# Optimization experiments

Measured on AMD Instinct MI355X. Metric: run time of the kernel, lower is better.

## Reference

```python
import jax, jax.numpy as jnp
import numpy as np
import math

K = 3
PAD = K // 2
C = 128          # out_channels
IN_CH = 256      # in_channels (concat of x2 and upsampled x1)
MOD_CH = 512     # modul_channels
SCALE = 1.0 / math.sqrt(C * K * K)


def conv2d(x, w, b=None, padding=0, groups=1):
    # x: [N, Cin, H, W], w: [Cout, Cin/groups, kh, kw]
    out = jax.lax.conv_general_dilated(
        x, w, window_strides=(1, 1),
        padding=[(padding, padding), (padding, padding)],
        feature_group_count=groups)
    if b is not None:
        out = out + b[None, :, None, None]
    return out


def leaky(x):
    return jnp.where(x >= 0, x, 0.1 * x)


def setup_inputs() -> dict:
    key = jax.random.key(0)
    ks = jax.random.split(key, 16)
    B, H, W = 8, 128, 128
    inp = {
        'x1': jax.random.normal(ks[0], (B, 128, H // 2, W // 2), jnp.float32),
        'x2': jax.random.normal(ks[1], (B, 128, H, W), jnp.float32),
        'xg': jax.random.normal(ks[2], (B, MOD_CH, 1, 1), jnp.float32),
        # modulation 1x1 conv
        'w_mod': jax.random.normal(ks[3], (C, MOD_CH, 1, 1), jnp.float32) * 0.05,
        'b_mod': jnp.ones((C,), jnp.float32),
        # styled weight parameter
        'w_style': jax.random.normal(ks[4], (1, C, C, K, K), jnp.float32),
        # ResBlock params
        'w_bottle': jax.random.normal(ks[5], (C, IN_CH, 1, 1), jnp.float32) * 0.05,
        'b_bottle': jnp.zeros((C,), jnp.float32),
        'w_dc1': jax.random.normal(ks[6], (C, C, 3, 3), jnp.float32) * 0.03,
        'b_dc1': jnp.zeros((C,), jnp.float32),
        'w_dc2': jax.random.normal(ks[7], (C, C, 3, 3), jnp.float32) * 0.03,
        'b_dc2': jnp.zeros((C,), jnp.float32),
        # conv_last
        'w_last': jax.random.normal(ks[8], (C, C, 3, 3), jnp.float32) * 0.03,
        'b_last': jnp.zeros((C,), jnp.float32),
    }
    return inp


def reference(x1, x2, xg, w_mod, b_mod, w_style, w_bottle, b_bottle,
              w_dc1, b_dc1, w_dc2, b_dc2, w_last, b_last):
    B, _, H, W = x2.shape
    # style modulation: [B, C, 1, 1] -> [B, 1, C, 1, 1]
    style = conv2d(xg, w_mod, b_mod).reshape(B, 1, C, 1, 1)
    weight = SCALE * w_style * style                         # [B, C, C, K, K]
    demod = jax.lax.rsqrt(jnp.sum(weight * weight, axis=(2, 3, 4)) + 1e-8)
    weight = weight * demod[:, :, None, None, None]
    weight = weight.reshape(B * C, C, K, K)
    x1u = jax.image.resize(x1, (B, x1.shape[1], H, W), method='bilinear')
    x = jnp.concatenate([x2, x1u], axis=1)                   # [B, IN_CH, H, W]
    # ResBlock
    x = conv2d(x, w_bottle, b_bottle)
    y = leaky(conv2d(x, w_dc1, b_dc1, padding=1))
    y = conv2d(y, w_dc2, b_dc2, padding=1)
    x = (y + x) / math.sqrt(2)
    # per-sample modulated grouped conv
    x_in = x.reshape(1, B * C, H, W)
    x_global = conv2d(x_in, weight, padding=PAD, groups=B).reshape(B, C, H, W)
    out = leaky(conv2d(x_global, w_last, b_last, padding=1))
    return out
```

## Files before the change

kernel.cpp:

```cpp
#include <hip/hip_runtime.h>
#include <stdint.h>

typedef _Float16 f16x8 __attribute__((ext_vector_type(8)));
typedef float    f32x4 __attribute__((ext_vector_type(4)));

#define DEVFN static __device__ __forceinline__

DEVFN unsigned short f2hu(float f) {
  _Float16 h = (_Float16)f;
  return __builtin_bit_cast(unsigned short, h);
}
DEVFN float h2f(unsigned short u) {
  return (float)__builtin_bit_cast(_Float16, u);
}
DEVFN float lrelu(float v) { return v >= 0.f ? v : 0.1f * v; }

DEVFN void gload16(const void* g, const void* l) {
  __builtin_amdgcn_global_load_lds(
      (const __attribute__((address_space(1))) void*)(uintptr_t)g,
      (__attribute__((address_space(3))) void*)(uint32_t)(uintptr_t)l,
      16, 0, 0);
}

static constexpr float SCALE_C = 0.029462782549439476f;

static constexpr size_t OFF_SIN  = 0;
static constexpr size_t OFF_DS   = 4096;
static constexpr size_t OFF_ZERO = 8192;
static constexpr size_t OFF_W2   = 12288;
static constexpr size_t OFF_WPK  = 77824;
static constexpr size_t OFF_WB   = OFF_WPK + 4ull * 147456ull * 2ull;
static constexpr size_t OFF_XCAT = OFF_WB + 65536;
static constexpr size_t OFF_XB   = OFF_XCAT + 8ull * 16384ull * 256ull * 2ull;
static constexpr size_t OFF_Y1   = OFF_XB + 8ull * 16384ull * 128ull * 2ull;

__global__ __launch_bounds__(256) void prep1_kernel(
    const float* __restrict__ xg, const float* __restrict__ w_mod,
    const float* __restrict__ b_mod, const float* __restrict__ w_style,
    const float* __restrict__ w_dc1, const float* __restrict__ w_dc2,
    const float* __restrict__ w_last, const float* __restrict__ w_bottle,
    unsigned short* __restrict__ wpk, unsigned short* __restrict__ wb,
    float* __restrict__ s_in, float* __restrict__ w2buf,
    float* __restrict__ zerob) {
  const int idx = (int)blockIdx.x * 256 + (int)threadIdx.x;
  if (idx < 589824) {
    const int t  = idx / 147456;
    const int e  = idx - t * 147456;
    const int co = e / 1152;
    const int r  = e - co * 1152;
    const int tap = r >> 7;
    const int ci  = r & 127;
    const float* src = (t == 0) ? w_dc1 : (t == 1) ? w_dc2 : (t == 2) ? w_style : w_last;
    wpk[idx] = f2hu(src[(size_t)(co * 128 + ci) * 9 + tap]);
    return;
  }
  int j = idx - 589824;
  if (j < 32768) { wb[j] = f2hu(w_bottle[j]); return; }
  j -= 32768;
  if (j < 65536) {
    const int pair = j >> 6, ln = j & 63;
    const int b = pair >> 7, ci = pair & 127;
    float st = 0.f;
    for (int m = ln; m < 512; m += 64) st += xg[b * 512 + m] * w_mod[ci * 512 + m];
    for (int off = 32; off > 0; off >>= 1) st += __shfl_down(st, off);
    if (ln == 0) s_in[pair] = st + b_mod[ci];
    return;
  }
  j -= 65536;
  if (j < 16384) {
    float acc = 0.f;
#pragma unroll
    for (int t = 0; t < 9; ++t) { float w = w_style[(size_t)j * 9 + t]; acc += w * w; }
    w2buf[j] = acc;
    return;
  }
  j -= 16384;
  if (j < 64) zerob[j] = 0.f;
}

__global__ __launch_bounds__(256) void prep2_kernel(
    const float* __restrict__ s_in, const float* __restrict__ w2buf,
    float* __restrict__ dscale) {
  const int j = (int)blockIdx.x * 256 + (int)threadIdx.x;
  const int pair = j >> 6, ln = j & 63;
  const int b = pair >> 7, co = pair & 127;
  const float s0 = s_in[b * 128 + ln];
  const float s1 = s_in[b * 128 + 64 + ln];
  float acc = s0 * s0 * w2buf[co * 128 + ln] + s1 * s1 * w2buf[co * 128 + 64 + ln];
  for (int off = 32; off > 0; off >>= 1) acc += __shfl_down(acc, off);
  if (ln == 0)
    dscale[pair] = SCALE_C * rsqrtf(SCALE_C * SCALE_C * acc + 1e-8f);
}

__global__ __launch_bounds__(256) void upcat_kernel(
    const float* __restrict__ x2, const float* __restrict__ x1,
    unsigned short* __restrict__ xcat) {
  __shared__ unsigned short lds[256 * 128];
  const int bid = (int)blockIdx.x;
  const int b = bid >> 7, h = bid & 127;
  const int tid = (int)threadIdx.x;
  const int crow = tid >> 5, wq = tid & 31;

  for (int it = 0; it < 16; ++it) {
    const int c = it * 8 + crow;
    const float4 v = *(const float4*)(x2 + ((size_t)(b * 128 + c) * 16384 + h * 128 + wq * 4));
    ushort4 u;
    u.x = f2hu(v.x); u.y = f2hu(v.y); u.z = f2hu(v.z); u.w = f2hu(v.w);
    *(ushort4*)(&lds[c * 128 + wq * 4]) = u;
  }
  const int m = h >> 1;
  const bool oddh = (h & 1);
  const int ly = oddh ? m : m - 1;
  const float fy = oddh ? 0.25f : 0.75f;
  const int y0 = ly < 0 ? 0 : ly;
  const int y1 = (ly + 1) > 63 ? 63 : (ly + 1);
  for (int it = 0; it < 16; ++it) {
    const int c = it * 8 + crow;
    const float* r0 = x1 + ((size_t)(b * 128 + c) * 4096 + y0 * 64);
    const float* r1 = x1 + ((size_t)(b * 128 + c) * 4096 + y1 * 64);
    ushort4 u;
    unsigned short* up = (unsigned short*)&u;
#pragma unroll
    for (int k = 0; k < 4; ++k) {
      const int w = wq * 4 + k;
      const int n = w >> 1;
      const bool oddw = (w & 1);
      const int lx = oddw ? n : n - 1;
      const float fx = oddw ? 0.25f : 0.75f;
      const int x0i = lx < 0 ? 0 : lx;
      const int x1i = (lx + 1) > 63 ? 63 : (lx + 1);
      const float vy0 = (1.f - fx) * r0[x0i] + fx * r0[x1i];
      const float vy1 = (1.f - fx) * r1[x0i] + fx * r1[x1i];
      up[k] = f2hu((1.f - fy) * vy0 + fy * vy1);
    }
    *(ushort4*)(&lds[(128 + c) * 128 + wq * 4]) = u;
  }
  __syncthreads();
  const int w = tid >> 1;
  const int c0 = (tid & 1) << 7;
  unsigned short* dst = xcat + ((size_t)((b * 128 + h) * 128 + w)) * 256 + c0;
  for (int i0 = 0; i0 < 128; i0 += 8) {
    unsigned int a0 = lds[(c0 + i0 + 0) * 128 + w];
    unsigned int a1 = lds[(c0 + i0 + 1) * 128 + w];
    unsigned int a2 = lds[(c0 + i0 + 2) * 128 + w];
    unsigned int a3 = lds[(c0 + i0 + 3) * 128 + w];
    unsigned int a4 = lds[(c0 + i0 + 4) * 128 + w];
    unsigned int a5 = lds[(c0 + i0 + 5) * 128 + w];
    unsigned int a6 = lds[(c0 + i0 + 6) * 128 + w];
    unsigned int a7 = lds[(c0 + i0 + 7) * 128 + w];
    uint4 q;
    q.x = a0 | (a1 << 16); q.y = a2 | (a3 << 16);
    q.z = a4 | (a5 << 16); q.w = a6 | (a7 << 16);
    *(uint4*)(dst + i0) = q;
  }
}

template <int TAPS, int CTOT, int EPI>
__global__ __launch_bounds__(512, 1) void conv_mfma(
    const unsigned short* __restrict__ Xin, const unsigned short* __restrict__ Wpk,
    const float* __restrict__ bias, const float* __restrict__ sstyle,
    const unsigned short* __restrict__ resid, unsigned short* __restrict__ outb,
    float* __restrict__ outf, const float* __restrict__ zerob) {
  constexpr int ROWS = (TAPS > 1) ? 4 : 2;
  constexpr int WSL  = (TAPS > 1) ? 130 : 128;
  constexpr int XSLOTS = ROWS * WSL * 4;
  constexpr int WSLOTS = 128 * TAPS * 4;
  constexpr int XBYTES = XSLOTS * 16;
  constexpr int NCB = CTOT / 32;

  __shared__ char smem[XBYTES + WSLOTS * 16];

  const int bid0 = (int)blockIdx.x;
  const int bid  = (bid0 & 7) * 64 + (bid0 >> 3);
  const int b  = bid >> 6;
  const int h0 = (bid & 63) << 1;

  const int tid = (int)threadIdx.x;
  const int wid = tid >> 6, lane = tid & 63;
  const int wm = wid >> 1, wn = wid & 1;
  const int g = lane >> 4, l15 = lane & 15;

  f32x4 acc[4][4] = {};

  const size_t imgbase = (size_t)b * 16384 * CTOT;

  for (int cb = 0; cb < NCB; ++cb) {
    const int ci0 = cb * 32;
    __syncthreads();
    for (int sb = wid * 64; sb < XSLOTS; sb += 512) {
      const int s = sb + lane;
      const int rws = s >> 2, cpr = s & 3;
      const int row = rws / WSL;
      const int ws  = rws - row * WSL;
      const int c   = cpr ^ (ws & 3);
      const void* src;
      if (TAPS > 1) {
        const int hrow = h0 + row - 1;
        const int w = ws - 1;
        src = (hrow >= 0 && hrow < 128 && w >= 0 && w < 128)
                  ? (const void*)(Xin + imgbase + (size_t)(hrow * 128 + w) * CTOT + ci0 + c * 8)
                  : (const void*)zerob;
      } else {
        src = Xin + imgbase + (size_t)((h0 + row) * 128 + ws) * CTOT + ci0 + c * 8;
      }
      if ((XSLOTS & 511) == 0 || s < XSLOTS) gload16(src, smem + sb * 16);
    }
    for (int sb = wid * 64; sb < WSLOTS; sb += 512) {
      const int s = sb + lane;
      const int co  = s / (TAPS * 4);
      const int rem = s - co * (TAPS * 4);
      const int tap = rem >> 2, cpr = rem & 3;
      const int c = cpr ^ (co & 3);
      gload16(Wpk + (size_t)(co * TAPS + tap) * CTOT + ci0 + c * 8,
              smem + XBYTES + sb * 16);
    }
    __syncthreads();
#pragma unroll
    for (int tap = 0; tap < TAPS; ++tap) {
      f16x8 af[4], bf[4];
#pragma unroll
      for (int mf = 0; mf < 4; ++mf) {
        const int mm = wm * 64 + mf * 16 + l15;
        const int r_out = mm >> 7, w = mm & 127;
        const int rrow = (TAPS > 1) ? (r_out + tap / 3) : r_out;
        const int ws   = (TAPS > 1) ? (w + tap % 3) : w;
        af[mf] = *(const f16x8*)(smem + ((rrow * WSL + ws) * 4 + (g ^ (ws & 3))) * 16);
      }
#pragma unroll
      for (int nf = 0; nf < 4; ++nf) {
        const int co = wn * 64 + nf * 16 + l15;
        bf[nf] = *(const f16x8*)(smem + XBYTES + ((co * TAPS + tap) * 4 + (g ^ (co & 3))) * 16);
      }
#pragma unroll
      for (int mf = 0; mf < 4; ++mf)
#pragma unroll
        for (int nf = 0; nf < 4; ++nf)
          acc[mf][nf] = __builtin_amdgcn_mfma_f32_16x16x32_f16(af[mf], bf[nf], acc[mf][nf], 0, 0, 0);
    }
  }

  const int hrow = h0 + (wm >> 1);
  const int wb0  = (wm & 1) * 64;
#pragma unroll
  for (int nf = 0; nf < 4; ++nf) {
    const int co = wn * 64 + nf * 16 + l15;
    float bv = 0.f;
    if (EPI == 0 || EPI == 1 || EPI == 2 || EPI == 4) bv = bias[co];
    float sv = 0.f;
    if (EPI == 2 || EPI == 3) sv = sstyle[b * 128 + co];
#pragma unroll
    for (int mf = 0; mf < 4; ++mf) {
      const int wcol = wb0 + mf * 16 + 4 * g;
      const f32x4 v = acc[mf][nf];
      if (EPI == 4) {
        float4 o;
        o.x = lrelu(v[0] + bv); o.y = lrelu(v[1] + bv);
        o.z = lrelu(v[2] + bv); o.w = lrelu(v[3] + bv);
        *(float4*)(outf + ((size_t)(b * 128 + co) * 16384 + hrow * 128 + wcol)) = o;
      } else {
#pragma unroll
        for (int r = 0; r < 4; ++r) {
          const size_t pidx = ((size_t)((b * 128 + hrow) * 128 + (wcol + r))) * 128 + co;
          float x = v[r];
          if (EPI == 0) x += bv;
          if (EPI == 1) x = lrelu(x + bv);
          if (EPI == 2) x = (x + bv + h2f(resid[pidx])) * 0.70710678118654752f * sv;
          if (EPI == 3) x *= sv;
          outb[pidx] = f2hu(x);
        }
      }
    }
  }
}

extern "C" void kernel_launch(void* const* d_in, const int* in_sizes, int n_in,
                              void* d_out, int out_size, void* d_ws, size_t ws_size,
                              hipStream_t stream) {
  (void)in_sizes; (void)n_in; (void)out_size; (void)ws_size;
  const float* x1       = (const float*)d_in[0];
  const float* x2       = (const float*)d_in[1];
  const float* xg       = (const float*)d_in[2];
  const float* w_mod    = (const float*)d_in[3];
  const float* b_mod    = (const float*)d_in[4];
  const float* w_style  = (const float*)d_in[5];
  const float* w_bottle = (const float*)d_in[6];
  const float* b_bottle = (const float*)d_in[7];
  const float* w_dc1    = (const float*)d_in[8];
  const float* b_dc1    = (const float*)d_in[9];
  const float* w_dc2    = (const float*)d_in[10];
  const float* b_dc2    = (const float*)d_in[11];
  const float* w_last   = (const float*)d_in[12];
  const float* b_last   = (const float*)d_in[13];
  float* out = (float*)d_out;

  char* ws = (char*)d_ws;
  float* s_in           = (float*)(ws + OFF_SIN);
  float* dscale         = (float*)(ws + OFF_DS);
  float* zerob          = (float*)(ws + OFF_ZERO);
  float* w2buf          = (float*)(ws + OFF_W2);
  unsigned short* wpk   = (unsigned short*)(ws + OFF_WPK);
  unsigned short* wb    = (unsigned short*)(ws + OFF_WB);
  unsigned short* xcat  = (unsigned short*)(ws + OFF_XCAT);
  unsigned short* xb    = (unsigned short*)(ws + OFF_XB);
  unsigned short* y1    = (unsigned short*)(ws + OFF_Y1);
  unsigned short* xr    = xcat;
  unsigned short* xglob = xb;

  prep1_kernel<<<2753, 256, 0, stream>>>(xg, w_mod, b_mod, w_style, w_dc1, w_dc2,
                                         w_last, w_bottle, wpk, wb, s_in, w2buf, zerob);
  prep2_kernel<<<256, 256, 0, stream>>>(s_in, w2buf, dscale);
  upcat_kernel<<<1024, 256, 0, stream>>>(x2, x1, xcat);
  conv_mfma<1, 256, 0><<<512, 512, 0, stream>>>(xcat, wb, b_bottle, nullptr, nullptr, xb, nullptr, zerob);
  conv_mfma<9, 128, 1><<<512, 512, 0, stream>>>(xb, wpk, b_dc1, nullptr, nullptr, y1, nullptr, zerob);
  conv_mfma<9, 128, 2><<<512, 512, 0, stream>>>(y1, wpk + 147456, b_dc2, s_in, xb, xr, nullptr, zerob);
  conv_mfma<9, 128, 3><<<512, 512, 0, stream>>>(xr, wpk + 2 * 147456, nullptr, dscale, nullptr, xglob, nullptr, zerob);
  conv_mfma<9, 128, 4><<<512, 512, 0, stream>>>(xglob, wpk + 3 * 147456, b_last, nullptr, nullptr, nullptr, out, zerob);
}
```

Measured before the change: 423.3 us.

## Double-buffer conv input tiles, enlarge row tiles, stream weights from global

The conv kernel now processes four output rows per block (256 blocks) and double-buffers the input tile in LDS. The next channel block is prefetched with global_load_lds while MFMAs run on the current one, using explicit vmcnt waits and barriers. For 3x3 convs, weights are read straight from global/cache into registers instead of being staged in LDS; the 1x1 bottleneck preloads its full weight matrix into LDS once. The upsample/concat kernel is split into half-width tiles with a padded transpose buffer. The extra overlap and reuse aim to hide load latency, at the cost of hand-tuned waitcnt counts, higher register pressure and only 256 blocks.

```diff
diff --git a/kernel.cpp b/kernel.cpp
--- a/kernel.cpp
+++ b/kernel.cpp
@@ -75,7 +75,7 @@
     return;
   }
   j -= 16384;
-  if (j < 64) zerob[j] = 0.f;
+  if (j < 128) zerob[j] = 0.f;
 }
 
 __global__ __launch_bounds__(256) void prep2_kernel(
@@ -92,175 +92,203 @@
     dscale[pair] = SCALE_C * rsqrtf(SCALE_C * SCALE_C * acc + 1e-8f);
 }
 
-__global__ __launch_bounds__(256) void upcat_kernel(
+__global__ __launch_bounds__(256) void upcat2_kernel(
     const float* __restrict__ x2, const float* __restrict__ x1,
     unsigned short* __restrict__ xcat) {
-  __shared__ unsigned short lds[256 * 128];
+  __shared__ unsigned short lt[256][65];
   const int bid = (int)blockIdx.x;
-  const int b = bid >> 7, h = bid & 127;
+  const int b = bid >> 8, h = (bid >> 1) & 127, w0 = (bid & 1) << 6;
   const int tid = (int)threadIdx.x;
-  const int crow = tid >> 5, wq = tid & 31;
-
-  for (int it = 0; it < 16; ++it) {
-    const int c = it * 8 + crow;
-    const float4 v = *(const float4*)(x2 + ((size_t)(b * 128 + c) * 16384 + h * 128 + wq * 4));
-    ushort4 u;
-    u.x = f2hu(v.x); u.y = f2hu(v.y); u.z = f2hu(v.z); u.w = f2hu(v.w);
-    *(ushort4*)(&lds[c * 128 + wq * 4]) = u;
+  const int cr = tid >> 4, wq = tid & 15;
+
+#pragma unroll
+  for (int p = 0; p < 8; ++p) {
+    const int c = p * 16 + cr;
+    const float4 v = *(const float4*)(x2 + ((size_t)(b * 128 + c) * 16384 + h * 128 + w0 + wq * 4));
+    lt[c][wq * 4 + 0] = f2hu(v.x);
+    lt[c][wq * 4 + 1] = f2hu(v.y);
+    lt[c][wq * 4 + 2] = f2hu(v.z);
+    lt[c][wq * 4 + 3] = f2hu(v.w);
   }
   const int m = h >> 1;
-  const bool oddh = (h & 1);
-  const int ly = oddh ? m : m - 1;
-  const float fy = oddh ? 0.25f : 0.75f;
+  const bool oh = (h & 1);
+  const int ly = oh ? m : m - 1;
+  const float fy = oh ? 0.25f : 0.75f;
   const int y0 = ly < 0 ? 0 : ly;
   const int y1 = (ly + 1) > 63 ? 63 : (ly + 1);
-  for (int it = 0; it < 16; ++it) {
-    const int c = it * 8 + crow;
+#pragma unroll
+  for (int p = 0; p < 8; ++p) {
+    const int c = p * 16 + cr;
     const float* r0 = x1 + ((size_t)(b * 128 + c) * 4096 + y0 * 64);
     const float* r1 = x1 + ((size_t)(b * 128 + c) * 4096 + y1 * 64);
-    ushort4 u;
-    unsigned short* up = (unsigned short*)&u;
 #pragma unroll
     for (int k = 0; k < 4; ++k) {
-      const int w = wq * 4 + k;
+      const int w = w0 + wq * 4 + k;
       const int n = w >> 1;
-      const bool oddw = (w & 1);
-      const int lx = oddw ? n : n - 1;
-      const float fx = oddw ? 0.25f : 0.75f;
+      const bool ow = (w & 1);
+      const int lx = ow ? n : n - 1;
+      const float fx = ow ? 0.25f : 0.75f;
       const int x0i = lx < 0 ? 0 : lx;
       const int x1i = (lx + 1) > 63 ? 63 : (lx + 1);
       const float vy0 = (1.f - fx) * r0[x0i] + fx * r0[x1i];
       const float vy1 = (1.f - fx) * r1[x0i] + fx * r1[x1i];
-      up[k] = f2hu((1.f - fy) * vy0 + fy * vy1);
-    }
-    *(ushort4*)(&lds[(128 + c) * 128 + wq * 4]) = u;
+      lt[128 + c][wq * 4 + k] = f2hu((1.f - fy) * vy0 + fy * vy1);
+    }
   }
   __syncthreads();
-  const int w = tid >> 1;
-  const int c0 = (tid & 1) << 7;
-  unsigned short* dst = xcat + ((size_t)((b * 128 + h) * 128 + w)) * 256 + c0;
-  for (int i0 = 0; i0 < 128; i0 += 8) {
-    unsigned int a0 = lds[(c0 + i0 + 0) * 128 + w];
-    unsigned int a1 = lds[(c0 + i0 + 1) * 128 + w];
-    unsigned int a2 = lds[(c0 + i0 + 2) * 128 + w];
-    unsigned int a3 = lds[(c0 + i0 + 3) * 128 + w];
-    unsigned int a4 = lds[(c0 + i0 + 4) * 128 + w];
-    unsigned int a5 = lds[(c0 + i0 + 5) * 128 + w];
-    unsigned int a6 = lds[(c0 + i0 + 6) * 128 + w];
-    unsigned int a7 = lds[(c0 + i0 + 7) * 128 + w];
-    uint4 q;
-    q.x = a0 | (a1 << 16); q.y = a2 | (a3 << 16);
-    q.z = a4 | (a5 << 16); q.w = a6 | (a7 << 16);
-    *(uint4*)(dst + i0) = q;
+  const int cp = tid & 31, pr = tid >> 5;
+  unsigned int* outp = (unsigned int*)(xcat + ((size_t)((b * 128 + h) * 128 + w0)) * 256);
+#pragma unroll
+  for (int cpass = 0; cpass < 4; ++cpass) {
+    const int c = cpass * 64 + cp * 2;
+#pragma unroll
+    for (int pp = 0; pp < 8; ++pp) {
+      const int wl = pp * 8 + pr;
+      const unsigned int val = (unsigned int)lt[c][wl] | ((unsigned int)lt[c + 1][wl] << 16);
+      outp[(size_t)wl * 128 + (c >> 1)] = val;
+    }
   }
 }
 
 template <int TAPS, int CTOT, int EPI>
-__global__ __launch_bounds__(512, 1) void conv_mfma(
-    const unsigned short* __restrict__ Xin, const unsigned short* __restrict__ Wpk,
+__global__ __launch_bounds__(512, 2) void conv2_mfma(
+    const char* __restrict__ wsb, uint32_t xoff,
+    const unsigned short* __restrict__ wgl,
     const float* __restrict__ bias, const float* __restrict__ sstyle,
     const unsigned short* __restrict__ resid, unsigned short* __restrict__ outb,
-    float* __restrict__ outf, const float* __restrict__ zerob) {
-  constexpr int ROWS = (TAPS > 1) ? 4 : 2;
+    float* __restrict__ outf) {
+  constexpr int ROWS = (TAPS > 1) ? 6 : 4;
   constexpr int WSL  = (TAPS > 1) ? 130 : 128;
-  constexpr int XSLOTS = ROWS * WSL * 4;
-  constexpr int WSLOTS = 128 * TAPS * 4;
-  constexpr int XBYTES = XSLOTS * 16;
-  constexpr int NCB = CTOT / 32;
-
-  __shared__ char smem[XBYTES + WSLOTS * 16];
+  constexpr int XS   = ROWS * WSL * 4;
+  constexpr int SPT  = (XS + 511) / 512;
+  constexpr int XBP  = SPT * 512 * 16;
+  constexpr int NCB  = CTOT / 32;
+  constexpr int MF   = (TAPS > 1) ? 16 : 8;
+  constexpr int NF   = (TAPS > 1) ? 2 : 4;
+  constexpr int MTW  = (TAPS > 1) ? 256 : 128;
+  constexpr int LDSZ = 2 * XBP + ((TAPS > 1) ? 0 : 65536);
+
+  __shared__ char smem[LDSZ];
 
   const int bid0 = (int)blockIdx.x;
-  const int bid  = (bid0 & 7) * 64 + (bid0 >> 3);
-  const int b  = bid >> 6;
-  const int h0 = (bid & 63) << 1;
-
-  const int tid = (int)threadIdx.x;
-  const int wid = tid >> 6, lane = tid & 63;
-  const int wm = wid >> 1, wn = wid & 1;
-  const int g = lane >> 4, l15 = lane & 15;
-
-  f32x4 acc[4][4] = {};
-
-  const size_t imgbase = (size_t)b * 16384 * CTOT;
-
-  for (int cb = 0; cb < NCB; ++cb) {
-    const int ci0 = cb * 32;
-    __syncthreads();
-    for (int sb = wid * 64; sb < XSLOTS; sb += 512) {
-      const int s = sb + lane;
+  const int bid  = (bid0 & 7) * 32 + (bid0 >> 3);
+  const int b    = bid >> 5;
+  const int h0   = (bid & 31) << 2;
+
+  const int tid  = (int)threadIdx.x;
+  const int wid  = tid >> 6, lane = tid & 63;
+  const int wm   = (TAPS > 1) ? (wid >> 2) : (wid >> 1);
+  const int wn   = (TAPS > 1) ? (wid & 3) : (wid & 1);
+  const int g    = lane >> 4, l15 = lane & 15;
+
+  uint32_t offs[SPT];
+#pragma unroll
+  for (int i = 0; i < SPT; ++i) {
+    const int s = tid + i * 512;
+    uint32_t off = (uint32_t)OFF_ZERO;
+    if (s < XS) {
       const int rws = s >> 2, cpr = s & 3;
       const int row = rws / WSL;
       const int ws  = rws - row * WSL;
       const int c   = cpr ^ (ws & 3);
-      const void* src;
       if (TAPS > 1) {
-        const int hrow = h0 + row - 1;
-        const int w = ws - 1;
-        src = (hrow >= 0 && hrow < 128 && w >= 0 && w < 128)
-                  ? (const void*)(Xin + imgbase + (size_t)(hrow * 128 + w) * CTOT + ci0 + c * 8)
-                  : (const void*)zerob;
+        const int hr = h0 + row - 1, w = ws - 1;
+        if (hr >= 0 && hr < 128 && w >= 0 && w < 128)
+          off = xoff + (uint32_t)(((b * 16384 + hr * 128 + w) * CTOT) + c * 8) * 2u;
       } else {
-        src = Xin + imgbase + (size_t)((h0 + row) * 128 + ws) * CTOT + ci0 + c * 8;
-      }
-      if ((XSLOTS & 511) == 0 || s < XSLOTS) gload16(src, smem + sb * 16);
-    }
-    for (int sb = wid * 64; sb < WSLOTS; sb += 512) {
-      const int s = sb + lane;
-      const int co  = s / (TAPS * 4);
-      const int rem = s - co * (TAPS * 4);
-      const int tap = rem >> 2, cpr = rem & 3;
-      const int c = cpr ^ (co & 3);
-      gload16(Wpk + (size_t)(co * TAPS + tap) * CTOT + ci0 + c * 8,
-              smem + XBYTES + sb * 16);
-    }
-    __syncthreads();
+        off = xoff + (uint32_t)(((b * 16384 + (h0 + row) * 128 + ws) * CTOT) + c * 8) * 2u;
+      }
+    }
+    offs[i] = off;
+  }
+
+  if (TAPS == 1) {
+#pragma unroll
+    for (int i = 0; i < 8; ++i) {
+      const int s = tid + i * 512;
+      const int co = s >> 5;
+      const int c  = (s & 31) ^ (co & 31);
+      gload16(wgl + (co * 256 + c * 8), smem + 2 * XBP + (wid * 64 + i * 512) * 16);
+    }
+  }
+#pragma unroll
+  for (int i = 0; i < SPT; ++i)
+    gload16(wsb + offs[i], smem + (wid * 64 + i * 512) * 16);
+
+  f32x4 acc[MF][NF] = {};
+
+  for (int cb = 0; cb < NCB; ++cb) {
+    const int cur = cb & 1;
+    if (cb + 1 < NCB) {
+#pragma unroll
+      for (int i = 0; i < SPT; ++i) {
+        offs[i] += 64;
+        gload16(wsb + offs[i], smem + (cur ^ 1) * XBP + (wid * 64 + i * 512) * 16);
+      }
+      __builtin_amdgcn_sched_barrier(0);
+      if (TAPS > 1) asm volatile("s_waitcnt vmcnt(7)" ::: "memory");
+      else          asm volatile("s_waitcnt vmcnt(4)" ::: "memory");
+    } else {
+      __builtin_amdgcn_sched_barrier(0);
+      asm volatile("s_waitcnt vmcnt(0)" ::: "memory");
+    }
+    __builtin_amdgcn_sched_barrier(0);
+    __builtin_amdgcn_s_barrier();
+    __builtin_amdgcn_sched_barrier(0);
+
+    const char* xb = smem + cur * XBP;
+    const int ci0 = cb * 32;
 #pragma unroll
     for (int tap = 0; tap < TAPS; ++tap) {
-      f16x8 af[4], bf[4];
-#pragma unroll
-      for (int mf = 0; mf < 4; ++mf) {
-        const int mm = wm * 64 + mf * 16 + l15;
-        const int r_out = mm >> 7, w = mm & 127;
-        const int rrow = (TAPS > 1) ? (r_out + tap / 3) : r_out;
-        const int ws   = (TAPS > 1) ? (w + tap % 3) : w;
-        af[mf] = *(const f16x8*)(smem + ((rrow * WSL + ws) * 4 + (g ^ (ws & 3))) * 16);
-      }
-#pragma unroll
-      for (int nf = 0; nf < 4; ++nf) {
-        const int co = wn * 64 + nf * 16 + l15;
-        bf[nf] = *(const f16x8*)(smem + XBYTES + ((co * TAPS + tap) * 4 + (g ^ (co & 3))) * 16);
-      }
-#pragma unroll
-      for (int mf = 0; mf < 4; ++mf)
-#pragma unroll
-        for (int nf = 0; nf < 4; ++nf)
-          acc[mf][nf] = __builtin_amdgcn_mfma_f32_16x16x32_f16(af[mf], bf[nf], acc[mf][nf], 0, 0, 0);
-    }
-  }
-
-  const int hrow = h0 + (wm >> 1);
-  const int wb0  = (wm & 1) * 64;
-#pragma unroll
-  for (int nf = 0; nf < 4; ++nf) {
-    const int co = wn * 64 + nf * 16 + l15;
+      const int ty = tap / 3, tx = tap - ty * 3;
+      f16x8 bfr[NF];
+#pragma unroll
+      for (int nf = 0; nf < NF; ++nf) {
+        const int co = wn * (NF * 16) + nf * 16 + l15;
+        if (TAPS > 1)
+          bfr[nf] = *(const f16x8*)(wgl + (co * TAPS + tap) * CTOT + ci0 + g * 8);
+        else
+          bfr[nf] = *(const f16x8*)(smem + 2 * XBP + ((co * 32) + ((4 * cb + g) ^ (co & 31))) * 16);
+      }
+#pragma unroll
+      for (int mf = 0; mf < MF; ++mf) {
+        const int mm = wm * MTW + mf * 16 + l15;
+        const int ro = mm >> 7, w = mm & 127;
+        const int rr = (TAPS > 1) ? (ro + ty) : ro;
+        const int ws = (TAPS > 1) ? (w + tx) : w;
+        const f16x8 a = *(const f16x8*)(xb + ((rr * WSL + ws) * 4 + (g ^ (ws & 3))) * 16);
+#pragma unroll
+        for (int nf = 0; nf < NF; ++nf)
+          acc[mf][nf] = __builtin_amdgcn_mfma_f32_16x16x32_f16(a, bfr[nf], acc[mf][nf], 0, 0, 0);
+      }
+    }
+    __builtin_amdgcn_sched_barrier(0);
+    __builtin_amdgcn_s_barrier();
+    __builtin_amdgcn_sched_barrier(0);
+  }
+
+#pragma unroll
+  for (int nf = 0; nf < NF; ++nf) {
+    const int co = wn * (NF * 16) + nf * 16 + l15;
     float bv = 0.f;
-    if (EPI == 0 || EPI == 1 || EPI == 2 || EPI == 4) bv = bias[co];
+    if (EPI != 3) bv = bias[co];
     float sv = 0.f;
     if (EPI == 2 || EPI == 3) sv = sstyle[b * 128 + co];
 #pragma unroll
-    for (int mf = 0; mf < 4; ++mf) {
-      const int wcol = wb0 + mf * 16 + 4 * g;
+    for (int mf = 0; mf < MF; ++mf) {
+      const int pb = wm * MTW + mf * 16 + 4 * g;
+      const int hrow = h0 + (pb >> 7);
+      const int w = pb & 127;
       const f32x4 v = acc[mf][nf];
       if (EPI == 4) {
         float4 o;
         o.x = lrelu(v[0] + bv); o.y = lrelu(v[1] + bv);
         o.z = lrelu(v[2] + bv); o.w = lrelu(v[3] + bv);
-        *(float4*)(outf + ((size_t)(b * 128 + co) * 16384 + hrow * 128 + wcol)) = o;
+        *(float4*)(outf + ((size_t)(b * 128 + co) * 16384 + hrow * 128 + w)) = o;
       } else {
 #pragma unroll
         for (int r = 0; r < 4; ++r) {
-          const size_t pidx = ((size_t)((b * 128 + hrow) * 128 + (wcol + r))) * 128 + co;
+          const size_t pidx = ((size_t)((b * 128 + hrow) * 128 + (w + r))) * 128 + co;
           float x = v[r];
           if (EPI == 0) x += bv;
           if (EPI == 1) x = lrelu(x + bv);
@@ -303,16 +331,19 @@
   unsigned short* xcat  = (unsigned short*)(ws + OFF_XCAT);
   unsigned short* xb    = (unsigned short*)(ws + OFF_XB);
   unsigned short* y1    = (unsigned short*)(ws + OFF_Y1);
-  unsigned short* xr    = xcat;
-  unsigned short* xglob = xb;
 
   prep1_kernel<<<2753, 256, 0, stream>>>(xg, w_mod, b_mod, w_style, w_dc1, w_dc2,
                                          w_last, w_bottle, wpk, wb, s_in, w2buf, zerob);
   prep2_kernel<<<256, 256, 0, stream>>>(s_in, w2buf, dscale);
-  upcat_kernel<<<1024, 256, 0, stream>>>(x2, x1, xcat);
-  conv_mfma<1, 256, 0><<<512, 512, 0, stream>>>(xcat, wb, b_bottle, nullptr, nullptr, xb, nullptr, zerob);
-  conv_mfma<9, 128, 1><<<512, 512, 0, stream>>>(xb, wpk, b_dc1, nullptr, nullptr, y1, nullptr, zerob);
-  conv_mfma<9, 128, 2><<<512, 512, 0, stream>>>(y1, wpk + 147456, b_dc2, s_in, xb, xr, nullptr, zerob);
-  conv_mfma<9, 128, 3><<<512, 512, 0, stream>>>(xr, wpk + 2 * 147456, nullptr, dscale, nullptr, xglob, nullptr, zerob);
-  conv_mfma<9, 128, 4><<<512, 512, 0, stream>>>(xglob, wpk + 3 * 147456, b_last, nullptr, nullptr, nullptr, out, zerob);
-}
+  upcat2_kernel<<<2048, 256, 0, stream>>>(x2, x1, xcat);
+  conv2_mfma<1, 256, 0><<<256, 512, 0, stream>>>(ws, (uint32_t)OFF_XCAT, wb, b_bottle,
+                                                 nullptr, nullptr, xb, nullptr);
+  conv2_mfma<9, 128, 1><<<256, 512, 0, stream>>>(ws, (uint32_t)OFF_XB, wpk, b_dc1,
+                                                 nullptr, nullptr, y1, nullptr);
+  conv2_mfma<9, 128, 2><<<256, 512, 0, stream>>>(ws, (uint32_t)OFF_Y1, wpk + 147456, b_dc2,
+                                                 s_in, xb, xcat, nullptr);
+  conv2_mfma<9, 128, 3><<<256, 512, 0, stream>>>(ws, (uint32_t)OFF_XCAT, wpk + 2 * 147456, nullptr,
+                                                 dscale, nullptr, xb, nullptr);
+  conv2_mfma<9, 128, 4><<<256, 512, 0, stream>>>(ws, (uint32_t)OFF_XB, wpk + 3 * 147456, b_last,
+                                                 nullptr, nullptr, nullptr, out);
+}
```

Result: slower. 999.1 us (+136.0%).
